# Optimization experiments

Measured on AMD Instinct MI355X. Metric: run time of the kernel, lower is better.

The kernel has to match this reference:

```python
import jax, jax.numpy as jnp
import numpy as np


def compute_intervals(samples, L):
    """Build per-node [lower, upper) intervals for a complete binary tree.
    samples: (dim, 2^L - 1) betas, node j's beta splits its interval.
    Returns lowers, uppers: (dim, 2^L - 1), nodes in breadth-first order.
    Mirrors Tree.get_intervals: left child = [lo, lo + b*len],
    right child = [lo + b*len, lo + b*len + (1-b)*len].
    """
    dim = samples.shape[0]
    lo = jnp.zeros((dim, 1), samples.dtype)
    hi = jnp.ones((dim, 1), samples.dtype)
    lows, his = [lo], [hi]
    for l in range(L - 1):
        b = samples[:, 2**l - 1: 2**(l + 1) - 1]  # betas of level-l nodes (dim, 2^l)
        length = hi - lo
        split = lo + b * length
        right_hi = split + (1.0 - b) * length
        # children of node n are 2n+1 (left), 2n+2 (right) -> interleave
        lo = jnp.stack([lo, split], axis=-1).reshape(dim, -1)
        hi = jnp.stack([split, right_hi], axis=-1).reshape(dim, -1)
        lows.append(lo)
        his.append(hi)
    return jnp.concatenate(lows, axis=1), jnp.concatenate(his, axis=1)


def setup_inputs() -> dict:
    key = jax.random.key(0)
    k1, k2 = jax.random.split(key)
    n, dim, L = 1000000, 16, 8
    # points strictly inside (0,1) so the root interval (0,1] contains all of them
    x = jax.random.uniform(k1, (n, dim), jnp.float32, 1e-4, 1.0 - 1e-4)
    # sampled betas (stand-in for Beta(shapes,scales).rsample()), bounded away from 0/1
    samples = jax.random.uniform(k2, (dim, 2**L - 1), jnp.float32, 0.05, 0.95)
    return {"x": x, "samples": samples, "L": L}


def reference(x, samples, L):
    n, dim = x.shape
    lowers, uppers = compute_intervals(samples, L)  # (dim, n_nodes)
    loT, hiT, bT = lowers.T, uppers.T, samples.T    # (n_nodes, dim)
    d = jnp.arange(dim)[None, :]                    # (1, dim)
    idx = jnp.zeros((n, dim), jnp.int32)            # current node per (point, dim)
    log_y = jnp.zeros((n, dim), x.dtype)
    # Tree descent replaces the original's dense (n, dim, 2^L-1) containment
    # mask + nonzero + retry loop; the path visits exactly L nodes per (point, dim).
    for l in range(L):
        b = bT[idx, d]                              # (n, dim) beta at current node
        log_y = log_y + jnp.log(b)                  # prod of betas along path (in log)
        if l < L - 1:
            lo = loT[idx, d]
            hi = hiT[idx, d]
            split = lo + b * (hi - lo)
            # original containment: lower < x <= upper, so x <= split -> left child
            idx = jnp.where(x <= split, 2 * idx + 1, 2 * idx + 2)
    leaf_len = hiT[idx, d] - loT[idx, d]            # B at the leaf node
    return (log_y - jnp.log(leaf_len)).mean(axis=-1)  # (n,)
```

## Files before the change

kernel.cpp:

```cpp
#include <hip/hip_runtime.h>
#include <math.h>


constexpr int DIMS     = 16;
constexpr int NODES    = 255;
constexpr int INTERNAL = 127;
constexpr int LSTRIDE  = 128;

__global__ void build_luts(const float* __restrict__ samples,
                           float* __restrict__ split_lut,
                           float* __restrict__ value_lut)
{
#pragma clang fp contract(off)
    int t = blockIdx.x * blockDim.x + threadIdx.x;
    if (t >= DIMS * NODES) return;
    int d = t / NODES;
    int j = t - d * NODES;
    const float* s = samples + d * NODES;

    unsigned key = (unsigned)(j + 1);
    int level = 31 - __clz(key);
    float lo = 0.0f, hi = 1.0f, acc = 0.0f;
    int i = 0;
    for (int tb = level - 1; tb >= 0; --tb) {
        float b = s[i];
        acc += logf(b);
        float len = hi - lo;
        float split = lo + b * len;
        unsigned bit = (key >> tb) & 1u;
        if (bit == 0u) {
            hi = split;
        } else {
            lo = split;
            hi = split + (1.0f - b) * len;
        }
        i = 2 * i + 1 + (int)bit;
    }
    float b = s[j];
    if (j < INTERNAL) {
        float len = hi - lo;
        split_lut[d * LSTRIDE + j] = lo + b * len;
    } else {
        acc += logf(b);
        value_lut[d * LSTRIDE + (j - INTERNAL)] = acc - logf(hi - lo);
    }
}

__global__ __launch_bounds__(256) void polya_eval(
    const float* __restrict__ x,
    const float* __restrict__ split_lut,
    const float* __restrict__ value_lut,
    float* __restrict__ out,
    int n)
{
    __shared__ float s_split[DIMS * LSTRIDE];
    __shared__ float s_value[DIMS * LSTRIDE];
    for (int i = threadIdx.x; i < DIMS * LSTRIDE; i += 256) {
        s_split[i] = split_lut[i];
        s_value[i] = value_lut[i];
    }
    __syncthreads();

    const int stride = gridDim.x * 256;
    for (int p = blockIdx.x * 256 + threadIdx.x; p < n; p += stride) {
        const float4* xr = reinterpret_cast<const float4*>(x + (size_t)p * DIMS);
        float4 a = xr[0], b4 = xr[1], c = xr[2], e = xr[3];
        float xs[DIMS] = {a.x, a.y, a.z, a.w,  b4.x, b4.y, b4.z, b4.w,
                          c.x, c.y, c.z, c.w,  e.x,  e.y,  e.z,  e.w};
        float acc = 0.0f;
#pragma unroll
        for (int d = 0; d < DIMS; ++d) {
            const float xv = xs[d];
            int idx = 0;
#pragma unroll
            for (int l = 0; l < 7; ++l) {
                float sp = s_split[d * LSTRIDE + idx];
                idx = 2 * idx + 1 + (int)(xv > sp);
            }
            acc += s_value[d * LSTRIDE + (idx - INTERNAL)];
        }
        out[p] = acc * 0.0625f;
    }
}

extern "C" void kernel_launch(void* const* d_in, const int* in_sizes, int n_in,
                              void* d_out, int out_size, void* d_ws, size_t ws_size,
                              hipStream_t stream) {
    const float* x       = (const float*)d_in[0];
    const float* samples = (const float*)d_in[1];
    float* out = (float*)d_out;
    const int n = in_sizes[0] / DIMS;

    float* split_lut = (float*)d_ws;
    float* value_lut = split_lut + DIMS * LSTRIDE;

    build_luts<<<(DIMS * NODES + 255) / 256, 256, 0, stream>>>(samples, split_lut, value_lut);

    int blocks = (n + 255) / 256;
    if (blocks > 2048) blocks = 2048;
    polya_eval<<<blocks, 256, 0, stream>>>(x, split_lut, value_lut, out, n);
}
```

Baseline: 33.00 us.

## Fuse LUT construction into the evaluation kernel, dropping the separate launch

Removes the standalone build_luts kernel. Each block of the evaluation kernel now rebuilds the split and value lookup tables directly into shared memory from the samples array. This cuts one kernel launch and the global round-trip for the tables. In exchange, every one of up to 2048 blocks repeats 4080 node computations, each with a serial descent loop and logf calls, before it can start evaluating points.

```diff
diff --git a/kernel.cpp b/kernel.cpp
--- a/kernel.cpp
+++ b/kernel.cpp
@@ -7,20 +7,11 @@
 constexpr int INTERNAL = 127;
 constexpr int LSTRIDE  = 128;
 
-__global__ void build_luts(const float* __restrict__ samples,
-                           float* __restrict__ split_lut,
-                           float* __restrict__ value_lut)
-{
+__device__ void node_lohi(const float* s, int j, float& lo, float& hi, float& acc) {
 #pragma clang fp contract(off)
-    int t = blockIdx.x * blockDim.x + threadIdx.x;
-    if (t >= DIMS * NODES) return;
-    int d = t / NODES;
-    int j = t - d * NODES;
-    const float* s = samples + d * NODES;
-
     unsigned key = (unsigned)(j + 1);
     int level = 31 - __clz(key);
-    float lo = 0.0f, hi = 1.0f, acc = 0.0f;
+    lo = 0.0f; hi = 1.0f; acc = 0.0f;
     int i = 0;
     for (int tb = level - 1; tb >= 0; --tb) {
         float b = s[i];
@@ -28,45 +19,43 @@
         float len = hi - lo;
         float split = lo + b * len;
         unsigned bit = (key >> tb) & 1u;
-        if (bit == 0u) {
-            hi = split;
-        } else {
-            lo = split;
-            hi = split + (1.0f - b) * len;
-        }
+        if (bit == 0u) { hi = split; }
+        else { lo = split; hi = split + (1.0f - b) * len; }
         i = 2 * i + 1 + (int)bit;
-    }
-    float b = s[j];
-    if (j < INTERNAL) {
-        float len = hi - lo;
-        split_lut[d * LSTRIDE + j] = lo + b * len;
-    } else {
-        acc += logf(b);
-        value_lut[d * LSTRIDE + (j - INTERNAL)] = acc - logf(hi - lo);
     }
 }
 
-__global__ __launch_bounds__(256) void polya_eval(
+__global__ __launch_bounds__(256) void polya_fused(
     const float* __restrict__ x,
-    const float* __restrict__ split_lut,
-    const float* __restrict__ value_lut,
+    const float* __restrict__ samples,
     float* __restrict__ out,
     int n)
 {
+#pragma clang fp contract(off)
     __shared__ float s_split[DIMS * LSTRIDE];
     __shared__ float s_value[DIMS * LSTRIDE];
-    for (int i = threadIdx.x; i < DIMS * LSTRIDE; i += 256) {
-        s_split[i] = split_lut[i];
-        s_value[i] = value_lut[i];
+
+    for (int id = threadIdx.x; id < DIMS * NODES; id += 256) {
+        int d = id / NODES;
+        int j = id - d * NODES;
+        const float* s = samples + d * NODES;
+        float lo, hi, acc;
+        node_lohi(s, j, lo, hi, acc);
+        float b = s[j];
+        if (j < INTERNAL) {
+            s_split[d * LSTRIDE + j] = lo + b * (hi - lo);
+        } else {
+            s_value[d * LSTRIDE + (j - INTERNAL)] = acc + logf(b) - logf(hi - lo);
+        }
     }
     __syncthreads();
 
     const int stride = gridDim.x * 256;
     for (int p = blockIdx.x * 256 + threadIdx.x; p < n; p += stride) {
         const float4* xr = reinterpret_cast<const float4*>(x + (size_t)p * DIMS);
-        float4 a = xr[0], b4 = xr[1], c = xr[2], e = xr[3];
+        float4 a = xr[0], b4 = xr[1], c4 = xr[2], e4 = xr[3];
         float xs[DIMS] = {a.x, a.y, a.z, a.w,  b4.x, b4.y, b4.z, b4.w,
-                          c.x, c.y, c.z, c.w,  e.x,  e.y,  e.z,  e.w};
+                          c4.x, c4.y, c4.z, c4.w,  e4.x, e4.y, e4.z, e4.w};
         float acc = 0.0f;
 #pragma unroll
         for (int d = 0; d < DIMS; ++d) {
@@ -91,12 +80,7 @@
     float* out = (float*)d_out;
     const int n = in_sizes[0] / DIMS;
 
-    float* split_lut = (float*)d_ws;
-    float* value_lut = split_lut + DIMS * LSTRIDE;
-
-    build_luts<<<(DIMS * NODES + 255) / 256, 256, 0, stream>>>(samples, split_lut, value_lut);
-
     int blocks = (n + 255) / 256;
     if (blocks > 2048) blocks = 2048;
-    polya_eval<<<blocks, 256, 0, stream>>>(x, split_lut, value_lut, out, n);
+    polya_fused<<<blocks, 256, 0, stream>>>(x, samples, out, n);
 }
```

After: 69.69 us. 2.11x slower.
